# Kernel tuning notes

Measured on AMD Instinct MI355X. Metric: run time of the kernel, lower is better.

Reference implementation:

```python
import jax, jax.numpy as jnp
import numpy as np

N = 100000
E = 2000000
F = 64          # in_features == out_features (required by attention * h_j)
BETA = 0.5
NEG_SLOPE = 0.01  # torch F.leaky_relu default


def setup_inputs() -> dict:
    key = jax.random.key(0)
    k1, k2, k3, k4, k5, k6 = jax.random.split(key, 6)
    h = jax.random.normal(k1, (N, F), dtype=jnp.float32)
    adj = jax.random.randint(k2, (2, E), 0, N, dtype=jnp.int64)
    amount = jax.random.uniform(k3, (E,), dtype=jnp.float32)
    count = jax.random.uniform(k4, (E,), dtype=jnp.float32)
    fc_w = jax.random.normal(k5, (F, 2 * F), dtype=jnp.float32) * (1.0 / np.sqrt(2 * F))
    fc_b = jax.random.normal(k6, (F,), dtype=jnp.float32) * 0.01
    return {"h": h, "adj": adj, "amount": amount, "count": count,
            "fc_w": fc_w, "fc_b": fc_b}


def _minmax_norm(x):
    lo, hi = x.min(), x.max()
    return (x - lo) / (hi - lo + 1e-8)


def reference(h, adj, amount, count, fc_w, fc_b):
    # per-edge weight from normalized amount/count
    edge_weight = BETA * _minmax_norm(amount) + (1.0 - BETA) * _minmax_norm(count)  # [E]

    src, dst = adj[0], adj[1]
    h_i = h[src]                     # [E, F]
    h_j = h[dst]                     # [E, F]
    h_cat = jnp.concatenate([h_i, h_j], axis=1)  # [E, 2F]

    score = jnp.einsum('ef,of->eo', h_cat, fc_w) + fc_b  # [E, F_out]
    score = jnp.where(score >= 0, score, NEG_SLOPE * score)  # leaky_relu
    score = score * edge_weight[:, None]

    # softmax over ALL edges (dim 0), per feature, as in the original
    attention = jax.nn.softmax(score, axis=0)  # [E, F]

    agg = jnp.zeros_like(h).at[src].add(attention * h_j)  # scatter-add -> [N, F]
    return agg
```

## Files before the change

### kernel.cpp

```cpp
#include <hip/hip_runtime.h>
#include <hip/hip_fp16.h>
#include <math.h>

#define FDIM   64
#define NB     64
#define BSHIFT 6
#define BMASK  63
#define NBKT_AL 1792
#define EPTA   16
#define CHUNKA (EPTA * 256)
#define CAP    1792

__global__ __launch_bounds__(256) void count_mm_k(const int* __restrict__ src,
                                                  const float* __restrict__ amount,
                                                  const float* __restrict__ count,
                                                  int* __restrict__ ghist,
                                                  float4* __restrict__ partial,
                                                  int E, int nbkt) {
  __shared__ int lhist[NBKT_AL];
  __shared__ float4 lred[4];
  for (int k = threadIdx.x; k < nbkt; k += 256) lhist[k] = 0;
  __syncthreads();
  float amin = 3.4e38f, amax = -3.4e38f, cmin = 3.4e38f, cmax = -3.4e38f;
  int e0 = blockIdx.x * CHUNKA + threadIdx.x * EPTA;
  if (e0 + EPTA <= E) {
    #pragma unroll
    for (int q = 0; q < EPTA; q += 4) {
      int4   s4 = *(const int4*)(src + e0 + q);
      float4 a4 = *(const float4*)(amount + e0 + q);
      float4 c4 = *(const float4*)(count + e0 + q);
      atomicAdd(&lhist[s4.x >> BSHIFT], 1);
      atomicAdd(&lhist[s4.y >> BSHIFT], 1);
      atomicAdd(&lhist[s4.z >> BSHIFT], 1);
      atomicAdd(&lhist[s4.w >> BSHIFT], 1);
      amin = fminf(amin, fminf(fminf(a4.x, a4.y), fminf(a4.z, a4.w)));
      amax = fmaxf(amax, fmaxf(fmaxf(a4.x, a4.y), fmaxf(a4.z, a4.w)));
      cmin = fminf(cmin, fminf(fminf(c4.x, c4.y), fminf(c4.z, c4.w)));
      cmax = fmaxf(cmax, fmaxf(fmaxf(c4.x, c4.y), fmaxf(c4.z, c4.w)));
    }
  } else {
    for (int e = e0; e < E; e++) {
      atomicAdd(&lhist[src[e] >> BSHIFT], 1);
      float a = amount[e], c = count[e];
      amin = fminf(amin, a); amax = fmaxf(amax, a);
      cmin = fminf(cmin, c); cmax = fmaxf(cmax, c);
    }
  }
  #pragma unroll
  for (int off = 32; off; off >>= 1) {
    amin = fminf(amin, __shfl_down(amin, off));
    amax = fmaxf(amax, __shfl_down(amax, off));
    cmin = fminf(cmin, __shfl_down(cmin, off));
    cmax = fmaxf(cmax, __shfl_down(cmax, off));
  }
  if ((threadIdx.x & 63) == 0) lred[threadIdx.x >> 6] = make_float4(amin, amax, cmin, cmax);
  __syncthreads();
  for (int k = threadIdx.x; k < nbkt; k += 256)
    if (lhist[k]) atomicAdd(&ghist[k], lhist[k]);
  if (threadIdx.x == 0) {
    float4 r = lred[0];
    #pragma unroll
    for (int w = 1; w < 4; w++) {
      r.x = fminf(r.x, lred[w].x); r.y = fmaxf(r.y, lred[w].y);
      r.z = fminf(r.z, lred[w].z); r.w = fmaxf(r.w, lred[w].w);
    }
    partial[blockIdx.x] = r;
  }
}

__global__ __launch_bounds__(256) void scan2_k(const int* __restrict__ ghist,
                                               int* __restrict__ bktbase,
                                               int* __restrict__ cursor,
                                               int nbkt, int E,
                                               const float4* __restrict__ partial,
                                               float* __restrict__ mmf, int nb,
                                               double* __restrict__ colsum) {
  __shared__ int lds[256];
  int t = threadIdx.x;
  int running = 0;
  for (int c0 = 0; c0 < nbkt; c0 += 256) {
    int x = (c0 + t < nbkt) ? ghist[c0 + t] : 0;
    lds[t] = x; __syncthreads();
    for (int off = 1; off < 256; off <<= 1) {
      int v = (t >= off) ? lds[t - off] : 0;
      __syncthreads();
      lds[t] += v; __syncthreads();
    }
    if (c0 + t < nbkt) {
      int ex = running + lds[t] - x;
      bktbase[c0 + t] = ex;
      cursor[c0 + t] = ex;
    }
    running += lds[255];
    __syncthreads();
  }
  if (t == 0) bktbase[nbkt] = E;
  for (int i = t; i < 1024; i += 256) colsum[i] = 0.0;
  float amin = 3.4e38f, amax = -3.4e38f, cmin = 3.4e38f, cmax = -3.4e38f;
  for (int i = t; i < nb; i += 256) {
    float4 p = partial[i];
    amin = fminf(amin, p.x); amax = fmaxf(amax, p.y);
    cmin = fminf(cmin, p.z); cmax = fmaxf(cmax, p.w);
  }
  #pragma unroll
  for (int off = 32; off; off >>= 1) {
    amin = fminf(amin, __shfl_down(amin, off));
    amax = fmaxf(amax, __shfl_down(amax, off));
    cmin = fminf(cmin, __shfl_down(cmin, off));
    cmax = fmaxf(cmax, __shfl_down(cmax, off));
  }
  __shared__ float4 lred[4];
  if ((t & 63) == 0) lred[t >> 6] = make_float4(amin, amax, cmin, cmax);
  __syncthreads();
  if (t == 0) {
    float4 r = lred[0];
    #pragma unroll
    for (int w = 1; w < 4; w++) {
      r.x = fminf(r.x, lred[w].x); r.y = fmaxf(r.y, lred[w].y);
      r.z = fminf(r.z, lred[w].z); r.w = fmaxf(r.w, lred[w].w);
    }
    mmf[0] = r.x; mmf[1] = r.y; mmf[2] = r.z; mmf[3] = r.w;
  }
}

__global__ __launch_bounds__(256) void scatter_k(const int* __restrict__ src,
                                                 const int* __restrict__ dst,
                                                 const float* __restrict__ amount,
                                                 const float* __restrict__ count,
                                                 const float* __restrict__ mmf,
                                                 int* __restrict__ cursor,
                                                 int2* __restrict__ payload,
                                                 int E, int nbkt) {
  __shared__ int cntb[NBKT_AL];
  __shared__ int baseb[NBKT_AL];
  __shared__ int sbase[NBKT_AL];
  __shared__ int wsum[4];
  __shared__ int2 lpay[CHUNKA];
  __shared__ unsigned short lbkt[CHUNKA];
  const int t = threadIdx.x, blk = blockIdx.x;
  for (int k = t; k < nbkt; k += 256) cntb[k] = 0;
  __syncthreads();
  const float amin = mmf[0], amax = mmf[1], cmin = mmf[2], cmax = mmf[3];
  const float L2E = 1.4426950408889634f;
  const float ascale = 0.5f * L2E / (amax - amin + 1e-8f);
  const float cscale = 0.5f * L2E / (cmax - cmin + 1e-8f);
  int e0 = blk * CHUNKA + t * EPTA;
  const bool full = (e0 + EPTA <= E);
  int4 S[4]; int4 D[4]; float4 A[4]; float4 C[4];
  if (full) {
    #pragma unroll
    for (int q = 0; q < 4; q++) {
      S[q] = *(const int4*)(src + e0 + 4 * q);
      D[q] = *(const int4*)(dst + e0 + 4 * q);
      A[q] = *(const float4*)(amount + e0 + 4 * q);
      C[q] = *(const float4*)(count + e0 + 4 * q);
      atomicAdd(&cntb[S[q].x >> BSHIFT], 1);
      atomicAdd(&cntb[S[q].y >> BSHIFT], 1);
      atomicAdd(&cntb[S[q].z >> BSHIFT], 1);
      atomicAdd(&cntb[S[q].w >> BSHIFT], 1);
    }
  } else {
    for (int e = e0; e < E; e++) atomicAdd(&cntb[src[e] >> BSHIFT], 1);
  }
  __syncthreads();
  {
    const int wv = t >> 6, ln = t & 63;
    int carry = 0;
    #pragma unroll
    for (int c = 0; c < 7; c++) {
      int idx = wv * 448 + (c << 6) + ln;
      int x = (idx < nbkt) ? cntb[idx] : 0;
      int v = x;
      #pragma unroll
      for (int off = 1; off < 64; off <<= 1) {
        int u = __shfl_up(v, off);
        if (ln >= off) v += u;
      }
      if (idx < nbkt) baseb[idx] = carry + v - x;
      carry += __shfl(v, 63);
    }
    if (ln == 0) wsum[wv] = carry;
  }
  __syncthreads();
  {
    const int wv = t >> 6, ln = t & 63;
    int wpre = 0;
    #pragma unroll
    for (int i = 0; i < 4; i++) wpre += (i < wv) ? wsum[i] : 0;
    if (wpre) {
      #pragma unroll
      for (int c = 0; c < 7; c++) {
        int idx = wv * 448 + (c << 6) + ln;
        if (idx < nbkt) baseb[idx] += wpre;
      }
    }
  }
  __syncthreads();
  for (int k = t; k < nbkt; k += 256) {
    int cnt = cntb[k];
    if (cnt) sbase[k] = atomicAdd(&cursor[k], cnt);
    cntb[k] = baseb[k];
  }
  __syncthreads();
  auto ins = [&](int s, int d, float a, float c) {
    int b = s >> BSHIFT;
    float ew = (a - amin) * ascale + (c - cmin) * cscale;
    int pos = atomicAdd(&cntb[b], 1);
    lpay[pos] = make_int2((d << 8) | (s & BMASK), __float_as_int(ew));
    lbkt[pos] = (unsigned short)b;
  };
  if (full) {
    #pragma unroll
    for (int q = 0; q < 4; q++) {
      ins(S[q].x, D[q].x, A[q].x, C[q].x);
      ins(S[q].y, D[q].y, A[q].y, C[q].y);
      ins(S[q].z, D[q].z, A[q].z, C[q].z);
      ins(S[q].w, D[q].w, A[q].w, C[q].w);
    }
  } else {
    for (int e = e0; e < E; e++) ins(src[e], dst[e], amount[e], count[e]);
  }
  __syncthreads();
  const int ned = min(CHUNKA, E - blk * CHUNKA);
  for (int i = t; i < ned; i += 256) {
    int bk = lbkt[i];
    payload[sbase[bk] + (i - baseb[bk])] = lpay[i];
  }
}

__global__ __launch_bounds__(128) void pre_gemm(const float* __restrict__ h,
                                                const float* __restrict__ fc_w,
                                                const float* __restrict__ fc_b,
                                                float* __restrict__ G1,
                                                __half2* __restrict__ P, int N) {
  __shared__ float hs[NB * FDIM];
  const int t = threadIdx.x;
  const int o = t & 63, half = t >> 6;
  float w[FDIM];
  const float* wrow = fc_w + o * 128 + half * 64;
  #pragma unroll
  for (int f = 0; f < FDIM; f += 4) {
    float4 v = *(const float4*)(wrow + f);
    w[f] = v.x; w[f + 1] = v.y; w[f + 2] = v.z; w[f + 3] = v.w;
  }
  const float bias = (half == 0) ? fc_b[o] : 0.0f;
  const int n0 = blockIdx.x * NB;
  const int nrows = min(NB, N - n0);
  for (int i = t; i < nrows * FDIM; i += 128) hs[i] = h[(size_t)n0 * FDIM + i];
  __syncthreads();
  for (int n = 0; n < nrows; n++) {
    float4 a4 = make_float4(0.f, 0.f, 0.f, 0.f);
    #pragma unroll
    for (int f = 0; f < FDIM; f += 4) {
      float4 hv = *(const float4*)(&hs[n * FDIM + f]);
      a4.x += hv.x * w[f];
      a4.y += hv.y * w[f + 1];
      a4.z += hv.z * w[f + 2];
      a4.w += hv.w * w[f + 3];
    }
    float acc = (a4.x + a4.y) + (a4.z + a4.w) + bias;
    if (half == 0) {
      G1[(size_t)(n0 + n) * FDIM + o] = acc;
    } else {
      P[(size_t)(n0 + n) * FDIM + o] =
          __halves2half2(__float2half(acc), __float2half(hs[n * FDIM + o]));
    }
  }
}

__device__ __forceinline__ float2 unpack_h2(unsigned u) {
  __half2 v = *(__half2*)&u;
  return make_float2(__low2float(v), __high2float(v));
}

__global__ __launch_bounds__(256) void fusedB_k(const int2* __restrict__ payload,
                                                const int* __restrict__ bktbase,
                                                const float* __restrict__ G1,
                                                const unsigned* __restrict__ P,
                                                double* __restrict__ colsum,
                                                float* __restrict__ out,
                                                int E, int nbkt) {
  __shared__ int2 lpay[CAP];
  __shared__ int fcnt[64];
  __shared__ int fcur[64];
  __shared__ float part[256];
  const int b = blockIdx.x;
  const int t = threadIdx.x;
  const int lane = t & 63;
  const int wv = __builtin_amdgcn_readfirstlane(t >> 6);
  const int node0 = b << BSHIFT;
  const int base = bktbase[b];
  const int end  = bktbase[b + 1];
  const int nchunks = (end - base + CAP - 1) / CAP;
  const bool multi = (nchunks > 1);
  float csum = 0.0f;
  for (int c = 0; c < nchunks; c++) {
    const int cs = base + c * CAP;
    const int m = min(CAP, end - cs);
    if (t < 64) fcnt[t] = 0;
    __syncthreads();
    int2 myp0, myp1, myp2, myp3, myp4, myp5, myp6;
    {
      int i;
      i = t;        if (i < m) { myp0 = payload[cs + i]; atomicAdd(&fcnt[myp0.x & 63], 1); }
      i = t + 256;  if (i < m) { myp1 = payload[cs + i]; atomicAdd(&fcnt[myp1.x & 63], 1); }
      i = t + 512;  if (i < m) { myp2 = payload[cs + i]; atomicAdd(&fcnt[myp2.x & 63], 1); }
      i = t + 768;  if (i < m) { myp3 = payload[cs + i]; atomicAdd(&fcnt[myp3.x & 63], 1); }
      i = t + 1024; if (i < m) { myp4 = payload[cs + i]; atomicAdd(&fcnt[myp4.x & 63], 1); }
      i = t + 1280; if (i < m) { myp5 = payload[cs + i]; atomicAdd(&fcnt[myp5.x & 63], 1); }
      i = t + 1536; if (i < m) { myp6 = payload[cs + i]; atomicAdd(&fcnt[myp6.x & 63], 1); }
    }
    __syncthreads();
    if (wv == 0) {
      int x = fcnt[lane];
      int v = x;
      #pragma unroll
      for (int off = 1; off < 64; off <<= 1) {
        int u = __shfl_up(v, off);
        if (lane >= off) v += u;
      }
      fcur[lane] = v - x;
    }
    __syncthreads();
    {
      int i;
      i = t;        if (i < m) lpay[atomicAdd(&fcur[myp0.x & 63], 1)] = myp0;
      i = t + 256;  if (i < m) lpay[atomicAdd(&fcur[myp1.x & 63], 1)] = myp1;
      i = t + 512;  if (i < m) lpay[atomicAdd(&fcur[myp2.x & 63], 1)] = myp2;
      i = t + 768;  if (i < m) lpay[atomicAdd(&fcur[myp3.x & 63], 1)] = myp3;
      i = t + 1024; if (i < m) lpay[atomicAdd(&fcur[myp4.x & 63], 1)] = myp4;
      i = t + 1280; if (i < m) lpay[atomicAdd(&fcur[myp5.x & 63], 1)] = myp5;
      i = t + 1536; if (i < m) lpay[atomicAdd(&fcur[myp6.x & 63], 1)] = myp6;
    }
    __syncthreads();
    const int per = (((m + 3) >> 2) + 63) & ~63;
    const int ws = wv * per;
    const int we = min(ws + per, m);
    int curnode = -1;
    bool firstf = true;
    float acc = 0.0f, g1 = 0.0f;
    auto flush_to = [&](int node) {
      if (curnode >= 0) {
        float* dp = out + (size_t)curnode * FDIM + lane;
        if (multi || firstf) { atomicAdd(dp, acc); firstf = false; }
        else *dp = acc;
      }
      curnode = node; acc = 0.0f;
      g1 = G1[(size_t)node * FDIM + lane];
    };
    for (int c0 = ws; c0 < we; c0 += 64) {
      const int mm = min(64, we - c0);
      int2 p = make_int2(0, 0);
      if (lane < mm) p = lpay[c0 + lane];
      if (mm == 64) {
        #pragma unroll 1
        for (int j = 0; j < 64; j += 16) {
          int xs[16]; float ee[16]; unsigned uu[16];
          #pragma unroll
          for (int k = 0; k < 16; k++) {
            xs[k] = __builtin_amdgcn_readlane(p.x, j + k);
            ee[k] = __int_as_float(__builtin_amdgcn_readlane(p.y, j + k));
          }
          #pragma unroll
          for (int k = 0; k < 16; k++) {
            unsigned off = (((unsigned)xs[k]) & 0xFFFFFF00u) | ((unsigned)lane << 2);
            uu[k] = *(const unsigned*)((const char*)P + off);
          }
          #pragma unroll
          for (int k = 0; k < 16; k++) {
            int node = node0 + (xs[k] & 63);
            if (node != curnode) flush_to(node);
            float2 v = unpack_h2(uu[k]);
            float sc = g1 + v.x;
            sc = fmaxf(sc, 0.01f * sc);
            float x = exp2f(sc * ee[k]);
            csum += x;
            acc += x * v.y;
          }
        }
      } else {
        for (int j = 0; j < mm; j += 16) {
          const int rem = mm - j;
          int xs[16]; float ee[16]; unsigned uu[16];
          #pragma unroll
          for (int k = 0; k < 16; k++) {
            xs[k] = __builtin_amdgcn_readlane(p.x, j + k);
            ee[k] = __int_as_float(__builtin_amdgcn_readlane(p.y, j + k));
          }
          #pragma unroll
          for (int k = 0; k < 16; k++) {
            unsigned off = (((unsigned)xs[k]) & 0xFFFFFF00u) | ((unsigned)lane << 2);
            uu[k] = *(const unsigned*)((const char*)P + off);
          }
          #pragma unroll
          for (int k = 0; k < 16; k++) {
            if (k < rem) {
              int node = node0 + (xs[k] & 63);
              if (node != curnode) flush_to(node);
              float2 v = unpack_h2(uu[k]);
              float sc = g1 + v.x;
              sc = fmaxf(sc, 0.01f * sc);
              float x = exp2f(sc * ee[k]);
              csum += x;
              acc += x * v.y;
            }
          }
        }
      }
    }
    if (curnode >= 0) atomicAdd(out + (size_t)curnode * FDIM + lane, acc);
    __syncthreads();
  }
  part[t] = csum;
  __syncthreads();
  if (t < 64) {
    float tot = part[t] + part[t + 64] + part[t + 128] + part[t + 192];
    atomicAdd(&colsum[t * 16], (double)tot);
  }
}

__global__ __launch_bounds__(256) void scale_k(float4* __restrict__ out4,
                                               const double* __restrict__ colsum,
                                               int total4) {
  __shared__ float rinv_s[64];
  if (threadIdx.x < 64) rinv_s[threadIdx.x] = (float)(1.0 / colsum[threadIdx.x * 16]);
  __syncthreads();
  const float4* r4 = (const float4*)rinv_s;
  int idx = blockIdx.x * blockDim.x + threadIdx.x;
  int stride = gridDim.x * blockDim.x;
  for (int i = idx; i < total4; i += stride) {
    float4 v = out4[i];
    float4 r = r4[i & 15];
    v.x *= r.x; v.y *= r.y; v.z *= r.z; v.w *= r.w;
    out4[i] = v;
  }
}

extern "C" void kernel_launch(void* const* d_in, const int* in_sizes, int n_in,
                              void* d_out, int out_size, void* d_ws, size_t ws_size,
                              hipStream_t stream) {
  const float* h      = (const float*)d_in[0];
  const int*   adj    = (const int*)d_in[1];
  const float* amount = (const float*)d_in[2];
  const float* count  = (const float*)d_in[3];
  const float* fc_w   = (const float*)d_in[4];
  const float* fc_b   = (const float*)d_in[5];
  float* out = (float*)d_out;

  const int E = in_sizes[2];
  const int N = in_sizes[0] / FDIM;
  const int* src = adj;
  const int* dst = adj + E;
  const int nbkt  = (N + BMASK) >> BSHIFT;
  const int nblkA = (E + CHUNKA - 1) / CHUNKA;

  char* ws = (char*)d_ws;
  size_t off = 0;
  auto alloc = [&](size_t bytes) { void* p = ws + off; off += (bytes + 255) & ~(size_t)255; return p; };
  float*    G1      = (float*)alloc((size_t)N * FDIM * sizeof(float));
  __half2*  P       = (__half2*)alloc((size_t)N * FDIM * sizeof(__half2));
  int2*     payload = (int2*)alloc((size_t)E * sizeof(int2));
  int*      ghist   = (int*)alloc((size_t)NBKT_AL * sizeof(int));
  int*      bktbase = (int*)alloc((size_t)(NBKT_AL + 1) * sizeof(int));
  int*      cursor  = (int*)alloc((size_t)NBKT_AL * sizeof(int));
  float4*   mmpart  = (float4*)alloc((size_t)nblkA * sizeof(float4));
  double*   colsum  = (double*)alloc(1024 * sizeof(double));
  float*    mmf     = (float*)alloc(4 * sizeof(float));

  hipMemsetAsync(d_out, 0, (size_t)out_size * sizeof(float), stream);
  hipMemsetAsync(ghist, 0, (size_t)nbkt * sizeof(int), stream);
  count_mm_k<<<nblkA, 256, 0, stream>>>(src, amount, count, ghist, mmpart, E, nbkt);
  scan2_k<<<1, 256, 0, stream>>>(ghist, bktbase, cursor, nbkt, E, mmpart, mmf, nblkA, colsum);
  scatter_k<<<nblkA, 256, 0, stream>>>(src, dst, amount, count, mmf, cursor, payload, E, nbkt);
  pre_gemm<<<(N + NB - 1) / NB, 128, 0, stream>>>(h, fc_w, fc_b, G1, P, N);
  fusedB_k<<<nbkt, 256, 0, stream>>>(payload, bktbase, G1, (const unsigned*)P, colsum, out, E, nbkt);
  scale_k<<<1024, 256, 0, stream>>>((float4*)out, colsum, N * FDIM / 4);
}
```

Measured before the change: 306.4 us.

## Widen node buckets to 128 with 1024-thread aggregation blocks; drop output memset

Doubles the node-bucket width from 64 to 128 nodes and raises the chunk capacity. The aggregation kernel now runs 1024-thread blocks, so each block covers more edges with 16 waves and fewer multi-chunk passes. The separate memset of the output is removed; instead each block records which nodes ever received edges and zeroes only the nodes that got none. The trade-off is that correctness now depends on touched nodes being written without relying on a pre-zeroed buffer, and larger blocks with more shared memory may lower occupancy.

```diff
diff --git a/kernel.cpp b/kernel.cpp
--- a/kernel.cpp
+++ b/kernel.cpp
@@ -4,12 +4,11 @@
 
 #define FDIM   64
 #define NB     64
-#define BSHIFT 6
-#define BMASK  63
-#define NBKT_AL 1792
+#define BSHIFT 7
+#define BMASK  127
 #define EPTA   16
 #define CHUNKA (EPTA * 256)
-#define CAP    1792
+#define CAP    3072
 
 __global__ __launch_bounds__(256) void count_mm_k(const int* __restrict__ src,
                                                   const float* __restrict__ amount,
@@ -17,7 +16,7 @@
                                                   int* __restrict__ ghist,
                                                   float4* __restrict__ partial,
                                                   int E, int nbkt) {
-  __shared__ int lhist[NBKT_AL];
+  __shared__ int lhist[1024];
   __shared__ float4 lred[4];
   for (int k = threadIdx.x; k < nbkt; k += 256) lhist[k] = 0;
   __syncthreads();
@@ -131,9 +130,9 @@
                                                  int* __restrict__ cursor,
                                                  int2* __restrict__ payload,
                                                  int E, int nbkt) {
-  __shared__ int cntb[NBKT_AL];
-  __shared__ int baseb[NBKT_AL];
-  __shared__ int sbase[NBKT_AL];
+  __shared__ int cntb[1024];
+  __shared__ int baseb[1024];
+  __shared__ int sbase[1024];
   __shared__ int wsum[4];
   __shared__ int2 lpay[CHUNKA];
   __shared__ unsigned short lbkt[CHUNKA];
@@ -167,8 +166,8 @@
     const int wv = t >> 6, ln = t & 63;
     int carry = 0;
     #pragma unroll
-    for (int c = 0; c < 7; c++) {
-      int idx = wv * 448 + (c << 6) + ln;
+    for (int c = 0; c < 4; c++) {
+      int idx = (wv << 8) + (c << 6) + ln;
       int x = (idx < nbkt) ? cntb[idx] : 0;
       int v = x;
       #pragma unroll
@@ -189,8 +188,8 @@
     for (int i = 0; i < 4; i++) wpre += (i < wv) ? wsum[i] : 0;
     if (wpre) {
       #pragma unroll
-      for (int c = 0; c < 7; c++) {
-        int idx = wv * 448 + (c << 6) + ln;
+      for (int c = 0; c < 4; c++) {
+        int idx = (wv << 8) + (c << 6) + ln;
         if (idx < nbkt) baseb[idx] += wpre;
       }
     }
@@ -273,17 +272,18 @@
   return make_float2(__low2float(v), __high2float(v));
 }
 
-__global__ __launch_bounds__(256) void fusedB_k(const int2* __restrict__ payload,
-                                                const int* __restrict__ bktbase,
-                                                const float* __restrict__ G1,
-                                                const unsigned* __restrict__ P,
-                                                double* __restrict__ colsum,
-                                                float* __restrict__ out,
-                                                int E, int nbkt) {
+__global__ __launch_bounds__(1024) void fusedB_k(const int2* __restrict__ payload,
+                                                 const int* __restrict__ bktbase,
+                                                 const float* __restrict__ G1,
+                                                 const unsigned* __restrict__ P,
+                                                 double* __restrict__ colsum,
+                                                 float* __restrict__ out,
+                                                 int E, int nbkt, int N) {
   __shared__ int2 lpay[CAP];
-  __shared__ int fcnt[64];
-  __shared__ int fcur[64];
-  __shared__ float part[256];
+  __shared__ int fcnt[128];
+  __shared__ int fcur[128];
+  __shared__ int ever[128];
+  __shared__ float part[1024];
   const int b = blockIdx.x;
   const int t = threadIdx.x;
   const int lane = t & 63;
@@ -293,47 +293,47 @@
   const int end  = bktbase[b + 1];
   const int nchunks = (end - base + CAP - 1) / CAP;
   const bool multi = (nchunks > 1);
+  if (t < 128) ever[t] = 0;
   float csum = 0.0f;
   for (int c = 0; c < nchunks; c++) {
     const int cs = base + c * CAP;
     const int m = min(CAP, end - cs);
-    if (t < 64) fcnt[t] = 0;
-    __syncthreads();
-    int2 myp0, myp1, myp2, myp3, myp4, myp5, myp6;
+    if (t < 128) fcnt[t] = 0;
+    __syncthreads();
+    int2 myp0, myp1, myp2;
     {
       int i;
-      i = t;        if (i < m) { myp0 = payload[cs + i]; atomicAdd(&fcnt[myp0.x & 63], 1); }
-      i = t + 256;  if (i < m) { myp1 = payload[cs + i]; atomicAdd(&fcnt[myp1.x & 63], 1); }
-      i = t + 512;  if (i < m) { myp2 = payload[cs + i]; atomicAdd(&fcnt[myp2.x & 63], 1); }
-      i = t + 768;  if (i < m) { myp3 = payload[cs + i]; atomicAdd(&fcnt[myp3.x & 63], 1); }
-      i = t + 1024; if (i < m) { myp4 = payload[cs + i]; atomicAdd(&fcnt[myp4.x & 63], 1); }
-      i = t + 1280; if (i < m) { myp5 = payload[cs + i]; atomicAdd(&fcnt[myp5.x & 63], 1); }
-      i = t + 1536; if (i < m) { myp6 = payload[cs + i]; atomicAdd(&fcnt[myp6.x & 63], 1); }
-    }
-    __syncthreads();
+      i = t;        if (i < m) { myp0 = payload[cs + i]; atomicAdd(&fcnt[myp0.x & 127], 1); }
+      i = t + 1024; if (i < m) { myp1 = payload[cs + i]; atomicAdd(&fcnt[myp1.x & 127], 1); }
+      i = t + 2048; if (i < m) { myp2 = payload[cs + i]; atomicAdd(&fcnt[myp2.x & 127], 1); }
+    }
+    __syncthreads();
+    if (t < 128) ever[t] |= fcnt[t];
     if (wv == 0) {
-      int x = fcnt[lane];
-      int v = x;
+      int carry = 0;
       #pragma unroll
-      for (int off = 1; off < 64; off <<= 1) {
-        int u = __shfl_up(v, off);
-        if (lane >= off) v += u;
+      for (int cc = 0; cc < 2; cc++) {
+        int idx = (cc << 6) + lane;
+        int x = fcnt[idx];
+        int v = x;
+        #pragma unroll
+        for (int off = 1; off < 64; off <<= 1) {
+          int u = __shfl_up(v, off);
+          if (lane >= off) v += u;
+        }
+        fcur[idx] = carry + v - x;
+        carry += __shfl(v, 63);
       }
-      fcur[lane] = v - x;
     }
     __syncthreads();
     {
       int i;
-      i = t;        if (i < m) lpay[atomicAdd(&fcur[myp0.x & 63], 1)] = myp0;
-      i = t + 256;  if (i < m) lpay[atomicAdd(&fcur[myp1.x & 63], 1)] = myp1;
-      i = t + 512;  if (i < m) lpay[atomicAdd(&fcur[myp2.x & 63], 1)] = myp2;
-      i = t + 768;  if (i < m) lpay[atomicAdd(&fcur[myp3.x & 63], 1)] = myp3;
-      i = t + 1024; if (i < m) lpay[atomicAdd(&fcur[myp4.x & 63], 1)] = myp4;
-      i = t + 1280; if (i < m) lpay[atomicAdd(&fcur[myp5.x & 63], 1)] = myp5;
-      i = t + 1536; if (i < m) lpay[atomicAdd(&fcur[myp6.x & 63], 1)] = myp6;
-    }
-    __syncthreads();
-    const int per = (((m + 3) >> 2) + 63) & ~63;
+      i = t;        if (i < m) lpay[atomicAdd(&fcur[myp0.x & 127], 1)] = myp0;
+      i = t + 1024; if (i < m) lpay[atomicAdd(&fcur[myp1.x & 127], 1)] = myp1;
+      i = t + 2048; if (i < m) lpay[atomicAdd(&fcur[myp2.x & 127], 1)] = myp2;
+    }
+    __syncthreads();
+    const int per = (((m + 15) >> 4) + 63) & ~63;
     const int ws = wv * per;
     const int we = min(ws + per, m);
     int curnode = -1;
@@ -368,7 +368,7 @@
           }
           #pragma unroll
           for (int k = 0; k < 16; k++) {
-            int node = node0 + (xs[k] & 63);
+            int node = node0 + (xs[k] & 127);
             if (node != curnode) flush_to(node);
             float2 v = unpack_h2(uu[k]);
             float sc = g1 + v.x;
@@ -395,7 +395,7 @@
           #pragma unroll
           for (int k = 0; k < 16; k++) {
             if (k < rem) {
-              int node = node0 + (xs[k] & 63);
+              int node = node0 + (xs[k] & 127);
               if (node != curnode) flush_to(node);
               float2 v = unpack_h2(uu[k]);
               float sc = g1 + v.x;
@@ -411,10 +411,16 @@
     if (curnode >= 0) atomicAdd(out + (size_t)curnode * FDIM + lane, acc);
     __syncthreads();
   }
+  for (int nd = wv; nd < 128; nd += 16) {
+    if (ever[nd] == 0 && node0 + nd < N)
+      out[(size_t)(node0 + nd) * FDIM + lane] = 0.0f;
+  }
   part[t] = csum;
   __syncthreads();
   if (t < 64) {
-    float tot = part[t] + part[t + 64] + part[t + 128] + part[t + 192];
+    float tot = 0.0f;
+    #pragma unroll
+    for (int w = 0; w < 16; w++) tot += part[t + (w << 6)];
     atomicAdd(&colsum[t * 16], (double)tot);
   }
 }
@@ -460,19 +466,18 @@
   float*    G1      = (float*)alloc((size_t)N * FDIM * sizeof(float));
   __half2*  P       = (__half2*)alloc((size_t)N * FDIM * sizeof(__half2));
   int2*     payload = (int2*)alloc((size_t)E * sizeof(int2));
-  int*      ghist   = (int*)alloc((size_t)NBKT_AL * sizeof(int));
-  int*      bktbase = (int*)alloc((size_t)(NBKT_AL + 1) * sizeof(int));
-  int*      cursor  = (int*)alloc((size_t)NBKT_AL * sizeof(int));
+  int*      ghist   = (int*)alloc(1024 * sizeof(int));
+  int*      bktbase = (int*)alloc(1025 * sizeof(int));
+  int*      cursor  = (int*)alloc(1024 * sizeof(int));
   float4*   mmpart  = (float4*)alloc((size_t)nblkA * sizeof(float4));
   double*   colsum  = (double*)alloc(1024 * sizeof(double));
   float*    mmf     = (float*)alloc(4 * sizeof(float));
 
-  hipMemsetAsync(d_out, 0, (size_t)out_size * sizeof(float), stream);
   hipMemsetAsync(ghist, 0, (size_t)nbkt * sizeof(int), stream);
   count_mm_k<<<nblkA, 256, 0, stream>>>(src, amount, count, ghist, mmpart, E, nbkt);
   scan2_k<<<1, 256, 0, stream>>>(ghist, bktbase, cursor, nbkt, E, mmpart, mmf, nblkA, colsum);
   scatter_k<<<nblkA, 256, 0, stream>>>(src, dst, amount, count, mmf, cursor, payload, E, nbkt);
   pre_gemm<<<(N + NB - 1) / NB, 128, 0, stream>>>(h, fc_w, fc_b, G1, P, N);
-  fusedB_k<<<nbkt, 256, 0, stream>>>(payload, bktbase, G1, (const unsigned*)P, colsum, out, E, nbkt);
+  fusedB_k<<<nbkt, 1024, 0, stream>>>(payload, bktbase, G1, (const unsigned*)P, colsum, out, E, nbkt, N);
   scale_k<<<1024, 256, 0, stream>>>((float4*)out, colsum, N * FDIM / 4);
 }
```

Measured after the change: 318.3 us. 1.04x slower.
